# Kernel optimization log

Measured on AMD Instinct MI355X. Metric: run time of the kernel, lower is better.

Reference implementation:

```python
import jax, jax.numpy as jnp
import numpy as np

N = 100000   # n_entity
D = 128      # kg_emb_dim
R = 12       # n_relation
NB = 8       # num_bases
E = 1_000_000
P = 400_000  # hypergraph incidences
HE = 20_000  # hyperedges
B = 64       # users in batch
LR = 64      # related entities per hypergraph per user
LC = 32      # context entities per user
NH = 8       # mha heads
HD = D // NH


def setup_inputs() -> dict:
    key = jax.random.key(0)
    ks = jax.random.split(key, 32)
    s = 1.0 / np.sqrt(D)
    f = lambda i, shape, sc=s: jax.random.normal(ks[i], shape, dtype=jnp.float32) * sc
    ri = lambda i, shape, hi: jax.random.randint(ks[i], shape, 0, hi, dtype=jnp.int32)
    return {
        'entity_emb': f(0, (N, D)),
        'rgcn_bases': f(1, (NB, D, D)),
        'rgcn_comp': f(2, (R, NB)),
        'rgcn_root': f(3, (D, D)),
        'rgcn_bias': jnp.zeros((D,), jnp.float32),
        'sess_theta': f(4, (D, D)),
        'sess_bias': jnp.zeros((D,), jnp.float32),
        'know_theta': f(5, (D, D)),
        'know_bias': jnp.zeros((D,), jnp.float32),
        'in_proj_w': f(6, (3 * D, D)),
        'in_proj_b': jnp.zeros((3 * D,), jnp.float32),
        'out_proj_w': f(7, (D, D)),
        'out_proj_b': jnp.zeros((D,), jnp.float32),
        'attn_his_a': f(8, (D, D)),
        'attn_his_b': f(9, (D, 1)),
        'attn_a': f(10, (D, D)),
        'attn_b': f(11, (D, 1)),
        'rec_bias': jnp.zeros((N,), jnp.float32),
        'edge_src': ri(12, (E,), N),
        'edge_dst': ri(13, (E,), N),
        'edge_type': ri(14, (E,), R),
        'sess_nodes': ri(15, (P,), N),
        'sess_edges': ri(16, (P,), HE),
        'know_nodes': ri(17, (P,), N),
        'know_edges': ri(18, (P,), HE),
        'sess_rel_idx': ri(19, (B, LR), N),
        'know_rel_idx': ri(20, (B, LR), N),
        'context_idx': ri(21, (B, LC), N),
    }


def rgcn_conv(x, bases, comp, root, bias, src, dst, etype):
    # PyG RGCNConv with basis decomposition; per-relation mean aggregation
    # norm = 1/|N_r(i)| : count edges per (dst, relation)
    pair_key = dst * R + etype
    cnt = jax.ops.segment_sum(jnp.ones_like(src, dtype=x.dtype), pair_key, N * R)
    norm = 1.0 / jnp.maximum(cnt[pair_key], 1.0)  # [E]
    w = jnp.einsum('rb,bio->rio', comp, bases)    # [R, D, D]
    out = x @ root + bias
    for r in range(R):
        h_r = x @ w[r]                                            # [N, D]
        coef = norm * (etype == r).astype(x.dtype)                # [E]
        out = out + jax.ops.segment_sum(h_r[src] * coef[:, None], dst, N)
    return out


def hypergraph_conv(x, theta, bias, nodes, edges, n_hyperedges):
    # PyG HypergraphConv (no attention): D^-1 H W B^-1 H^T X Theta + bias
    xt = x @ theta                                                # [N, D]
    ones = jnp.ones(nodes.shape, x.dtype)
    b_deg = jax.ops.segment_sum(ones, edges, n_hyperedges)        # [HE]
    edge_feat = jax.ops.segment_sum(xt[nodes], edges, n_hyperedges)
    edge_feat = edge_feat * jnp.where(b_deg > 0, 1.0 / b_deg, 0.0)[:, None]
    d_deg = jax.ops.segment_sum(ones, nodes, N)                   # [N]
    out = jax.ops.segment_sum(edge_feat[edges], nodes, N)
    return out * jnp.where(d_deg > 0, 1.0 / d_deg, 0.0)[:, None] + bias


def self_attn_batch(h, a, b):
    # SelfAttentionBatch: e = tanh(h a) b; softmax over nodes; weighted sum
    e = jnp.einsum('bld,dk->blk', jnp.tanh(jnp.einsum('bld,de->ble', h, a)), b)[..., 0]
    attn = jax.nn.softmax(e, axis=-1)                             # [B, L]
    return jnp.einsum('bl,bld->bd', attn, h)


def mha(q, kv, in_proj_w, in_proj_b, out_proj_w, out_proj_b):
    # torch.nn.MultiheadAttention (batch_first) math
    wq, wk, wv = in_proj_w[:D], in_proj_w[D:2 * D], in_proj_w[2 * D:]
    bq, bk, bv = in_proj_b[:D], in_proj_b[D:2 * D], in_proj_b[2 * D:]
    qh = (q @ wq.T + bq).reshape(q.shape[0], q.shape[1], NH, HD)
    kh = (kv @ wk.T + bk).reshape(kv.shape[0], kv.shape[1], NH, HD)
    vh = (kv @ wv.T + bv).reshape(kv.shape[0], kv.shape[1], NH, HD)
    logits = jnp.einsum('bqhd,bkhd->bhqk', qh, kh) / np.sqrt(HD)
    attn = jax.nn.softmax(logits, axis=-1)
    o = jnp.einsum('bhqk,bkhd->bqhd', attn, vh).reshape(q.shape[0], q.shape[1], D)
    return o @ out_proj_w.T + out_proj_b


def reference(entity_emb, rgcn_bases, rgcn_comp, rgcn_root, rgcn_bias,
              sess_theta, sess_bias, know_theta, know_bias,
              in_proj_w, in_proj_b, out_proj_w, out_proj_b,
              attn_his_a, attn_his_b, attn_a, attn_b, rec_bias,
              edge_src, edge_dst, edge_type,
              sess_nodes, sess_edges, know_nodes, know_edges,
              sess_rel_idx, know_rel_idx, context_idx):
    # 1) RGCN over the full KG
    kg = rgcn_conv(entity_emb, rgcn_bases, rgcn_comp, rgcn_root, rgcn_bias,
                   edge_src, edge_dst, edge_type)
    # 2) session / knowledge hypergraph convolutions on RGCN output
    sess = hypergraph_conv(kg, sess_theta, sess_bias, sess_nodes, sess_edges, HE)
    know = hypergraph_conv(kg, know_theta, know_bias, know_nodes, know_edges, HE)
    # 3) per-user: related = concat(session_emb, knowledge_emb); context from kg
    related = jnp.concatenate([sess[sess_rel_idx], know[know_rel_idx]], axis=1)  # [B, 2LR, D]
    context = kg[context_idx]                                                    # [B, LC, D]
    # 4) MHItemAttention (context queries related) + gated attention pooling
    att_rel = mha(context, related, in_proj_w, in_proj_b, out_proj_w, out_proj_b)
    his = self_attn_batch(att_rel, attn_his_a, attn_his_b)                       # [B, D]
    user_cat = jnp.concatenate([context, his[:, None, :]], axis=1)               # [B, LC+1, D]
    user = self_attn_batch(user_cat, attn_a, attn_b)                             # [B, D]
    # 5) recommendation scores: F.linear(user, kg_embedding, rec_bias.bias)
    return user @ kg.T + rec_bias                                                # [B, N]
```

## Files before the change

kernel.cpp:

```cpp
#include <hip/hip_runtime.h>
#include <hip/hip_bf16.h>

#define DN 100000
#define DD 128
#define DR 12
#define DNB 8
#define DE 1000000
#define DP 400000
#define DHE 20000
#define DHE2 40000
#define DB 64
#define DLR 64
#define DLC 32
#define DNH 8
#define DHD 16
#define NRBINS (DR * DN)
#define SCAN_CHUNK 1024
#define MCAP 65536

typedef unsigned short ushortT;
typedef unsigned int uintT;
typedef __attribute__((ext_vector_type(8))) short s8v;
typedef __attribute__((ext_vector_type(4))) float f4v;

#define APAD 136

__device__ __forceinline__ ushortT rneb(float v) {
    uintT b = __float_as_uint(v);
    return (ushortT)((b + 0x7FFFu + ((b >> 16) & 1u)) >> 16);
}
__device__ __forceinline__ float b2f(ushortT h) {
    return __uint_as_float(((uintT)h) << 16);
}

__device__ __forceinline__ void split_store8(ushortT* hbase, ushortT* lbase, const float* v)
{
    ushortT h[8], l[8];
    #pragma unroll
    for (int j = 0; j < 8; ++j) {
        h[j] = rneb(v[j]);
        l[j] = rneb(v[j] - b2f(h[j]));
    }
    uint4 hv = make_uint4((uintT)h[0] | ((uintT)h[1] << 16), (uintT)h[2] | ((uintT)h[3] << 16),
                          (uintT)h[4] | ((uintT)h[5] << 16), (uintT)h[6] | ((uintT)h[7] << 16));
    uint4 lv = make_uint4((uintT)l[0] | ((uintT)l[1] << 16), (uintT)l[2] | ((uintT)l[3] << 16),
                          (uintT)l[4] | ((uintT)l[5] << 16), (uintT)l[6] | ((uintT)l[7] << 16));
    *(uint4*)hbase = hv;
    *(uint4*)lbase = lv;
}

__global__ __launch_bounds__(256) void k_presplit_all(
    const float* __restrict__ root, const float* __restrict__ st,
    const float* __restrict__ kt, const float* __restrict__ ipw,
    const float* __restrict__ opw, const float* __restrict__ aha,
    const float* __restrict__ aa, ushortT* __restrict__ outA)
{
    int gid = blockIdx.x * 256 + threadIdx.x;
    int mat = gid >> 14, e = gid & 16383;
    const float* srcs[9] = {root, st, kt, ipw, ipw + 16384, ipw + 32768, opw, aha, aa};
    const float* W = srcs[mat];
    bool t1 = (mat >= 3 && mat <= 6);
    int k = e & 31, n = (e >> 5) & 127, kc = e >> 12;
    float f = t1 ? W[(size_t)n * 128 + kc * 32 + k] : W[(size_t)(kc * 32 + k) * 128 + n];
    ushortT h = rneb(f);
    outA[(size_t)mat * 32768 + e] = h;
    outA[(size_t)mat * 32768 + 16384 + e] = rneb(f - b2f(h));
}

__global__ void k_wcomp_split(const float* __restrict__ comp, const float* __restrict__ bases,
                              ushortT* __restrict__ warena)
{
    int i = blockIdx.x * blockDim.x + threadIdx.x;
    if (i >= DR * DD * DD) return;
    int r = i / (DD * DD), io = i % (DD * DD);
    float s = 0.f;
    #pragma unroll
    for (int b = 0; b < DNB; ++b) s += comp[r * DNB + b] * bases[(size_t)b * DD * DD + io];
    int irow = io >> 7, o = io & 127;
    int kc = irow >> 5, k = irow & 31;
    size_t dst = (size_t)r * 32768 + (size_t)kc * 4096 + o * 32 + k;
    ushortT h = rneb(s);
    warena[dst] = h;
    warena[dst + 16384] = rneb(s - b2f(h));
}

__global__ __launch_bounds__(256) void k_gemm_ds(
    const float* __restrict__ A, const ushortT* __restrict__ Wb,
    const float* __restrict__ bias, const float* __restrict__ rs,
    const int* __restrict__ gidx, float* __restrict__ gout,
    float* __restrict__ C, int M)
{
    __shared__ __align__(16) ushortT Ah[64 * APAD], Al[64 * APAD];
    __shared__ __align__(16) ushortT Bs[8192];
    int tid = threadIdx.x;
    int row0 = blockIdx.x * 64;
    {
        int row = tid >> 2, c0 = (tid & 3) * 32;
        int gr = row0 + row;
        int arow = gr;
        if (gidx && gr < M) arow = gidx[gr];
        const float* ar = A + (size_t)arow * 128 + c0;
        float sc = 1.0f;
        if (rs && gr < M) { float d = rs[gr]; sc = (d > 0.f) ? 1.0f / d : 0.f; }
        #pragma unroll
        for (int g = 0; g < 4; ++g) {
            float v[8] = {};
            if (gr < M) {
                float4 u0 = *(const float4*)(ar + g * 8);
// ... 72 lines not shown
        }
    }
    f4v acc[8] = {};
    int w = tid >> 6, lane = tid & 63, m = lane & 15, quad = lane >> 4;
    for (int kc = 0; kc < 4; ++kc) {
        __syncthreads();
        {
            const ushortT* gh = Wb + kc * 4096;
            const ushortT* gl = Wb + 16384 + kc * 4096;
            *(s8v*)&Bs[tid * 8]        = *(const s8v*)&gh[tid * 8];
            *(s8v*)&Bs[2048 + tid * 8] = *(const s8v*)&gh[2048 + tid * 8];
            *(s8v*)&Bs[4096 + tid * 8] = *(const s8v*)&gl[tid * 8];
            *(s8v*)&Bs[6144 + tid * 8] = *(const s8v*)&gl[2048 + tid * 8];
        }
        __syncthreads();
        s8v ah = *(const s8v*)&Ah[(w * 16 + m) * APAD + kc * 32 + quad * 8];
        s8v al = *(const s8v*)&Al[(w * 16 + m) * APAD + kc * 32 + quad * 8];
        #pragma unroll
        for (int nt = 0; nt < 8; ++nt) {
            int boff = (nt * 16 + m) * 32 + quad * 8;
            s8v bh = *(const s8v*)&Bs[boff];
            s8v bl = *(const s8v*)&Bs[4096 + boff];
            acc[nt] = __builtin_amdgcn_mfma_f32_16x16x32_bf16(ah, bh, acc[nt], 0, 0, 0);
            acc[nt] = __builtin_amdgcn_mfma_f32_16x16x32_bf16(al, bh, acc[nt], 0, 0, 0);
            acc[nt] = __builtin_amdgcn_mfma_f32_16x16x32_bf16(ah, bl, acc[nt], 0, 0, 0);
        }
    }
    float bv[8];
    #pragma unroll
    for (int nt = 0; nt < 8; ++nt) bv[nt] = bvec[nt * 16 + m];
    #pragma unroll
    for (int rr = 0; rr < 4; ++rr) {
        float p = 0.f;
        #pragma unroll
        for (int nt = 0; nt < 8; ++nt) p += tanhf(acc[nt][rr]) * bv[nt];
        #pragma unroll
        for (int o = 1; o < 16; o <<= 1) p += __shfl_xor(p, o);
        int gr = row0 + w * 16 + quad * 4 + rr;
        if (m == 0 && gr < M) e[gr] = p;
    }
}

template <int L>
__global__ __launch_bounds__(128) void k_pool_apply(const float* __restrict__ h,
                                                    const float* __restrict__ e,
                                                    float* __restrict__ out,
                                                    ushortT* __restrict__ us)
{
    __shared__ float es[L];
    int b = blockIdx.x, tid = threadIdx.x;
    if (tid < L) es[tid] = e[b * L + tid];
    __syncthreads();
    float mx = -1e30f;
    #pragma unroll
    for (int l = 0; l < L; ++l) mx = fmaxf(mx, es[l]);
    float wgt[L];
    float sum = 0.f;
    #pragma unroll
    for (int l = 0; l < L; ++l) { wgt[l] = __expf(es[l] - mx); sum += wgt[l]; }
    float inv = 1.0f / sum;
    float o = 0.f;
    #pragma unroll
    for (int l = 0; l < L; ++l) o += wgt[l] * h[((size_t)b * L + l) * 128 + tid];
    float val = o * inv;
    out[(size_t)b * 128 + tid] = val;
    if (us) {
        ushortT hh = rneb(val);
        ushortT ll = rneb(val - b2f(hh));
        int e_ = ((tid >> 5) * 2048) + b * 32 + (tid & 31);
        us[e_] = hh;
        us[8192 + e_] = ll;
    }
}

__global__ void k_build_ucat(const float* __restrict__ ctx, const float* __restrict__ his,
                             float* ucat)
{
    int i = blockIdx.x * blockDim.x + threadIdx.x;
    if (i >= DB * 33 * 128) return;
    int d = i & 127, l = (i >> 7) % 33, b = i / (33 * 128);
    ucat[i] = (l < 32) ? ctx[((size_t)b * 32 + l) * 128 + d] : his[(size_t)b * 128 + d];
}

__global__ __launch_bounds__(256) void k_rgcn_all(
    const float* __restrict__ x, const ushortT* __restrict__ warena,
    const int* __restrict__ seglist, const int* __restrict__ soff,
    const int* __restrict__ slen, const int* __restrict__ ssrc,
    const int* __restrict__ stypebase, const int* __restrict__ bo,
    float* __restrict__ kg)
{
    __shared__ __align__(16) ushortT Ah[64 * APAD], Al[64 * APAD];
    __shared__ __align__(16) ushortT Bs[8192];
    int bid = blockIdx.x;
    if (bid >= bo[DR]) return;
    int r = 0;
    #pragma unroll 1
    while (bid >= bo[r + 1]) ++r;
    int s0 = stypebase[r], s1 = stypebase[r + 1];
    int base = s0 + (bid - bo[r]) * 64;
    int nrow = min(64, s1 - base);
    int tid = threadIdx.x;
    const ushortT* Wb = warena + (size_t)r * 32768;
    {
        int row = tid >> 2, c0 = (tid & 3) * 32;
        float a[32] = {};
        if (row < nrow) {
            int key = seglist[base + row];
            int len = slen[key];
            int st = soff[key] - len;
            for (int i = 0; i < len; ++i) {
                const float* xr = x + (size_t)ssrc[st + i] * 128 + c0;
                #pragma unroll
                for (int j = 0; j < 8; ++j) {
                    float4 v = *(const float4*)(xr + j * 4);
                    a[j*4+0] += v.x; a[j*4+1] += v.y; a[j*4+2] += v.z; a[j*4+3] += v.w;
                }
            }
            float inv = 1.0f / (float)max(len, 1);
            #pragma unroll
            for (int j = 0; j < 32; ++j) a[j] *= inv;
        }
        #pragma unroll
        for (int g = 0; g < 4; ++g)
            split_store8(&Ah[row * APAD + c0 + g * 8], &Al[row * APAD + c0 + g * 8], a + g * 8);
    }
    f4v acc[8] = {};
    int w = tid >> 6, lane = tid & 63, m = lane & 15, quad = lane >> 4;
    for (int kc = 0; kc < 4; ++kc) {
        __syncthreads();
        {
            const ushortT* gh = Wb + kc * 4096;
            const ushortT* gl = Wb + 16384 + kc * 4096;
            *(s8v*)&Bs[tid * 8]        = *(const s8v*)&gh[tid * 8];
            *(s8v*)&Bs[2048 + tid * 8] = *(const s8v*)&gh[2048 + tid * 8];
            *(s8v*)&Bs[4096 + tid * 8] = *(const s8v*)&gl[tid * 8];
            *(s8v*)&Bs[6144 + tid * 8] = *(const s8v*)&gl[2048 + tid * 8];
        }
        __syncthreads();
        s8v ah = *(const s8v*)&Ah[(w * 16 + m) * APAD + kc * 32 + quad * 8];
        s8v al = *(const s8v*)&Al[(w * 16 + m) * APAD + kc * 32 + quad * 8];
        #pragma unroll
        for (int nt = 0; nt < 8; ++nt) {
            int boff = (nt * 16 + m) * 32 + quad * 8;
            s8v bh = *(const s8v*)&Bs[boff];
            s8v bl = *(const s8v*)&Bs[4096 + boff];
            acc[nt] = __builtin_amdgcn_mfma_f32_16x16x32_bf16(ah, bh, acc[nt], 0, 0, 0);
            acc[nt] = __builtin_amdgcn_mfma_f32_16x16x32_bf16(al, bh, acc[nt], 0, 0, 0);
            acc[nt] = __builtin_amdgcn_mfma_f32_16x16x32_bf16(ah, bl, acc[nt], 0, 0, 0);
        }
    }
    #pragma unroll
    for (int rr = 0; rr < 4; ++rr) {
        int rt = w * 16 + quad * 4 + rr;
        if (rt < nrow) {
            int dst = seglist[base + rt] - r * DN;
            float* kr = kg + (size_t)dst * 128 + m;
            #pragma unroll
            for (int nt = 0; nt < 8; ++nt)
                atomicAdd(&kr[nt * 16], acc[nt][rr]);
        }
    }
}

__global__ __launch_bounds__(256) void k_score_ds(
    const float* __restrict__ kg, const ushortT* __restrict__ Ub,
    const float* __restrict__ rb, float* __restrict__ out)
{
    __shared__ __align__(16) ushortT Ah[64 * APAD], Al[64 * APAD];
    __shared__ __align__(16) ushortT Bs[4096];
    int tid = threadIdx.x;
    int n0 = blockIdx.x * 64;
    {
        int row = tid >> 2, c0 = (tid & 3) * 32;
        int gr = n0 + row;
        const float* ar = kg + (size_t)gr * 128 + c0;
        #pragma unroll
        for (int g = 0; g < 4; ++g) {
            float v[8] = {};
            if (gr < DN) {
                float4 u0 = *(const float4*)(ar + g * 8);
                float4 u1 = *(const float4*)(ar + g * 8 + 4);
                v[0]=u0.x; v[1]=u0.y; v[2]=u0.z; v[3]=u0.w;
                v[4]=u1.x; v[5]=u1.y; v[6]=u1.z; v[7]=u1.w;
            }
            split_store8(&Ah[row * APAD + c0 + g * 8], &Al[row * APAD + c0 + g * 8], v);
        }
    }
    f4v acc[4] = {};
    int w = tid >> 6, lane = tid & 63, m = lane & 15, quad = lane >> 4;
    for (int kc = 0; kc < 4; ++kc) {
        __syncthreads();
        {
            const ushortT* gh = Ub + kc * 2048;
            const ushortT* gl = Ub + 8192 + kc * 2048;
            *(s8v*)&Bs[tid * 8]        = *(const s8v*)&gh[tid * 8];
            *(s8v*)&Bs[2048 + tid * 8] = *(const s8v*)&gl[tid * 8];
        }
        __syncthreads();
        s8v ah = *(const s8v*)&Ah[(w * 16 + m) * APAD + kc * 32 + quad * 8];
        s8v al = *(const s8v*)&Al[(w * 16 + m) * APAD + kc * 32 + quad * 8];
        #pragma unroll
        for (int nt = 0; nt < 4; ++nt) {
            int boff = (nt * 16 + m) * 32 + quad * 8;
            s8v bh = *(const s8v*)&Bs[boff];
            s8v bl = *(const s8v*)&Bs[2048 + boff];
            acc[nt] = __builtin_amdgcn_mfma_f32_16x16x32_bf16(ah, bh, acc[nt], 0, 0, 0);
            acc[nt] = __builtin_amdgcn_mfma_f32_16x16x32_bf16(al, bh, acc[nt], 0, 0, 0);
            acc[nt] = __builtin_amdgcn_mfma_f32_16x16x32_bf16(ah, bl, acc[nt], 0, 0, 0);
        }
    }
    int n = n0 + w * 16 + quad * 4;
    if (n < DN) {
        float4 rbv = *(const float4*)&rb[n];
        #pragma unroll
        for (int nt = 0; nt < 4; ++nt) {
            int b = nt * 16 + m;
            float4 o = make_float4(acc[nt][0] + rbv.x, acc[nt][1] + rbv.y,
                                   acc[nt][2] + rbv.z, acc[nt][3] + rbv.w);
            *(float4*)&out[(size_t)b * DN + n] = o;
        }
    }
}

__global__ void k_scan_pass1(const int* __restrict__ in, int n, int* __restrict__ bsum)
{
    __shared__ int red[256];
    int b = blockIdx.x, t = threadIdx.x;
    int i0 = b * SCAN_CHUNK + t * 4;
    int s = 0;
    #pragma unroll
    for (int j = 0; j < 4; ++j) {
        int i = i0 + j;
        if (i < n) s += in[i];
    }
    red[t] = s;
    __syncthreads();
    for (int o = 128; o > 0; o >>= 1) {
        if (t < o) red[t] += red[t + o];
        __syncthreads();
    }
    if (t == 0) bsum[b] = red[0];
}

__global__ __launch_bounds__(256) void k_scan_pass2p(int* bsum, int nb, int* total)
{
    __shared__ int lds[256];
    __shared__ int carry;
    int t = threadIdx.x;
    if (t == 0) carry = 0;
    __syncthreads();
    for (int c0 = 0; c0 < nb; c0 += 256) {
        int i = c0 + t;
        int v = (i < nb) ? bsum[i] : 0;
        lds[t] = v;
        __syncthreads();
        for (int o = 1; o < 256; o <<= 1) {
            int add = (t >= o) ? lds[t - o] : 0;
            __syncthreads();
            lds[t] += add;
            __syncthreads();
        }
        int myc = carry;
        if (i < nb) bsum[i] = lds[t] - v + myc;
        int tot = lds[255];
        __syncthreads();
        if (t == 0) carry = myc + tot;
        __syncthreads();
    }
    if (total && t == 0) *total = carry;
}

__global__ void k_scan_pass3(const int* __restrict__ in, int n, const int* __restrict__ bsum,
                             int* __restrict__ out)
{
    __shared__ int lds[256];
    int b = blockIdx.x, t = threadIdx.x;
    int i0 = b * SCAN_CHUNK + t * 4;
    int v[4]; int s = 0;
    #pragma unroll
    for (int j = 0; j < 4; ++j) {
        int i = i0 + j;
        int x = 0;
        if (i < n) x = in[i];
        v[j] = x; s += x;
    }
    lds[t] = s;
    __syncthreads();
    for (int o = 1; o < 256; o <<= 1) {
        int add = (t >= o) ? lds[t - o] : 0;
        __syncthreads();
        lds[t] += add;
        __syncthreads();
    }
    int run = lds[t] - s + bsum[b];
    #pragma unroll
    for (int j = 0; j < 4; ++j) {
        int i = i0 + j;
        if (i < n) { out[i] = run; run += v[j]; }
    }
}

__global__ void k_scan2_pass1(const int* __restrict__ in, int n, int* bV, int* bP)
{
    __shared__ int redV[256], redP[256];
    int b = blockIdx.x, t = threadIdx.x;
    int i0 = b * SCAN_CHUNK + t * 4;
    int sv = 0, sp = 0;
    #pragma unroll
    for (int j = 0; j < 4; ++j) {
        int i = i0 + j;
        if (i < n) { int v = in[i]; sv += v; sp += (v > 0); }
    }
    redV[t] = sv; redP[t] = sp;
    __syncthreads();
    for (int o = 128; o > 0; o >>= 1) {
        if (t < o) { redV[t] += redV[t + o]; redP[t] += redP[t + o]; }
        __syncthreads();
    }
    if (t == 0) { bV[b] = redV[0]; bP[b] = redP[0]; }
}

__global__ __launch_bounds__(256) void k_scan2_pass2(int* bV, int* bP, int nb, int* totalP)
{
    __shared__ int lds[256];
    __shared__ int carry;
    int t = threadIdx.x;
    #pragma unroll 1
    for (int which = 0; which < 2; ++which) {
        int* bsum = which ? bP : bV;
        __syncthreads();
        if (t == 0) carry = 0;
        __syncthreads();
        for (int c0 = 0; c0 < nb; c0 += 256) {
            int i = c0 + t;
            int v = (i < nb) ? bsum[i] : 0;
            lds[t] = v;
            __syncthreads();
            for (int o = 1; o < 256; o <<= 1) {
                int add = (t >= o) ? lds[t - o] : 0;
                __syncthreads();
                lds[t] += add;
                __syncthreads();
            }
            int myc = carry;
            if (i < nb) bsum[i] = lds[t] - v + myc;
            int tot = lds[255];
            __syncthreads();
            if (t == 0) carry = myc + tot;
            __syncthreads();
        }
        if (which == 1 && totalP && t == 0) *totalP = carry;
    }
}

__global__ void k_scan2_pass3(const int* __restrict__ in, int n,
                              const int* __restrict__ bV, const int* __restrict__ bP,
                              int* __restrict__ outV, int* __restrict__ outP)
{
    __shared__ int ldsV[256], ldsP[256];
    int b = blockIdx.x, t = threadIdx.x;
    int i0 = b * SCAN_CHUNK + t * 4;
    int v[4]; int sv = 0, sp = 0;
    #pragma unroll
    for (int j = 0; j < 4; ++j) {
        int i = i0 + j;
        int x = 0;
        if (i < n) x = in[i];
        v[j] = x; sv += x; sp += (x > 0);
    }
    ldsV[t] = sv; ldsP[t] = sp;
    __syncthreads();
    for (int o = 1; o < 256; o <<= 1) {
        int addV = (t >= o) ? ldsV[t - o] : 0;
        int addP = (t >= o) ? ldsP[t - o] : 0;
        __syncthreads();
        ldsV[t] += addV; ldsP[t] += addP;
        __syncthreads();
    }
    int runV = ldsV[t] - sv + bV[b];
    int runP = ldsP[t] - sp + bP[b];
    #pragma unroll
    for (int j = 0; j < 4; ++j) {
        int i = i0 + j;
        if (i < n) {
            outV[i] = runV; outP[i] = runP;
            runV += v[j]; runP += (v[j] > 0);
        }
    }
}

__global__ void k_hist_both(const int* __restrict__ dst, const int* __restrict__ et,
                            int* __restrict__ hist,
                            const int* __restrict__ se, const int* __restrict__ ke,
                            int* __restrict__ hhist)
{
    int i = blockIdx.x * blockDim.x + threadIdx.x;
    if (i < DE) {
        atomicAdd(&hist[(size_t)et[i] * DN + dst[i]], 1);
    } else {
        int j = i - DE;
        if (j < DP) atomicAdd(&hhist[se[j]], 1);
        else if (j < 2 * DP) atomicAdd(&hhist[DHE + ke[j - DP]], 1);
    }
}

__global__ void k_seglist(const int* __restrict__ hist, const int* __restrict__ segpos,
                          int* __restrict__ seglist, int n)
{
    int i = blockIdx.x * blockDim.x + threadIdx.x;
    if (i < n && hist[i] > 0) seglist[segpos[i]] = i;
}

__global__ void k_stypebase(const int* __restrict__ segpos, int* stybase, int* bo)
{
    int t = threadIdx.x;
    if (t < DR) stybase[t] = segpos[(size_t)t * DN];
    if (t == 0) {
        int acc = 0; bo[0] = 0;
        int prev = segpos[0];
        for (int r = 0; r < DR; ++r) {
            int nxt = (r == DR - 1) ? stybase[DR] : segpos[(size_t)(r + 1) * DN];
            acc += (nxt - prev + 63) >> 6;
            bo[r + 1] = acc;
            prev = nxt;
        }
    }
}

__global__ void k_bucket_both(const int* __restrict__ src, const int* __restrict__ dst,
                              const int* __restrict__ et, int* __restrict__ soff,
                              int* __restrict__ ssrc,
                              const int* __restrict__ sn, const int* __restrict__ se,
                              const int* __restrict__ kn, const int* __restrict__ ke,
                              int* __restrict__ hoff, int* __restrict__ pns)
{
    int i = blockIdx.x * blockDim.x + threadIdx.x;
    if (i < DE) {
        int key = et[i] * DN + dst[i];
        int pos = atomicAdd(&soff[key], 1);
        ssrc[pos] = src[i];
    } else {
        int j = i - DE;
        if (j >= 2 * DP) return;
        int e, node;
        if (j < DP) { e = se[j]; node = sn[j]; }
        else { e = DHE + ke[j - DP]; node = kn[j - DP]; }
        int pos = atomicAdd(&hoff[e], 1);
        pns[pos] = node;
    }
}

__global__ void k_hyper_agg(const float* __restrict__ xsrc, const int* __restrict__ pns,
                            const int* __restrict__ hoff, const int* __restrict__ hcnt,
                            const int* __restrict__ heneed, float* __restrict__ efeat)
{
    int lane = threadIdx.x & 63;
    int he = (blockIdx.x * blockDim.x + threadIdx.x) >> 6;
    if (he >= DHE2) return;
    if (!heneed[he]) return;
    int len = hcnt[he];
    int st = hoff[he] - len;
    int half = lane >> 5;
    int c16 = (lane & 31) * 4;
    float4 acc = make_float4(0.f, 0.f, 0.f, 0.f);
    int c = 0;
    for (; c + 4 <= len; c += 4) {
        int n0 = pns[st + c + half];
        int n1 = pns[st + c + 2 + half];
        float4 v0 = *(const float4*)&xsrc[(size_t)n0 * 128 + c16];
        float4 v1 = *(const float4*)&xsrc[(size_t)n1 * 128 + c16];
        acc.x += v0.x + v1.x; acc.y += v0.y + v1.y;
        acc.z += v0.z + v1.z; acc.w += v0.w + v1.w;
    }
    for (; c < len; c += 2) {
        int idx = c + half;
        if (idx < len) {
            int n = pns[st + idx];
            float4 v = *(const float4*)&xsrc[(size_t)n * 128 + c16];
            acc.x += v.x; acc.y += v.y; acc.z += v.z; acc.w += v.w;
        }
    }
    acc.x += __shfl_xor(acc.x, 32);
    acc.y += __shfl_xor(acc.y, 32);
    acc.z += __shfl_xor(acc.z, 32);
    acc.w += __shfl_xor(acc.w, 32);
    if (half == 0) {
        float inv = (len > 0) ? 1.0f / (float)len : 0.f;
        float4 o = make_float4(acc.x * inv, acc.y * inv, acc.z * inv, acc.w * inv);
        *(float4*)&efeat[(size_t)he * 128 + c16] = o;
    }
}

__global__ void k_slot_assign2(const int* __restrict__ sidx, const int* __restrict__ kidx,
                               int* slot_s, int* slot_k, int* scnt)
{
    int i = blockIdx.x * blockDim.x + threadIdx.x;
    if (i < DB * DLR) {
        int node = sidx[i];
        if (atomicCAS(&slot_s[node], -1, -2) == -1) slot_s[node] = atomicAdd(&scnt[0], 1);
    } else if (i < 2 * DB * DLR) {
        int node = kidx[i - DB * DLR];
        if (atomicCAS(&slot_k[node], -1, -2) == -1) slot_k[node] = atomicAdd(&scnt[1], 1);
    }
}

__global__ __launch_bounds__(256) void k_sdeg_match(
    const int* __restrict__ nodes, const int* __restrict__ he, const int* __restrict__ slot,
    float* sdeg, int* mcnt, int* mhe, int* msl, int* heneed, int heBase)
{
    __shared__ int lcnt, lbase;
    if (threadIdx.x == 0) lcnt = 0;
    __syncthreads();
    int i = blockIdx.x * 256 + threadIdx.x;
    int s = -1, lidx = 0, h = 0;
    if (i < DP) {
        s = slot[nodes[i]];
        if (s >= 0) {
            h = heBase + he[i];
            heneed[h] = 1;
            atomicAdd(&sdeg[s], 1.0f);
            lidx = atomicAdd(&lcnt, 1);
        }
    }
    __syncthreads();
    if (threadIdx.x == 0) lbase = (lcnt > 0) ? atomicAdd(mcnt, lcnt) : 0;
    __syncthreads();
    if (s >= 0) {
        int idx = lbase + lidx;
        if (idx < MCAP) { mhe[idx] = h; msl[idx] = s; }
    }
}

__global__ void k_accmatch2(const float* __restrict__ efeat,
                            const int* __restrict__ mhe_s, const int* __restrict__ msl_s,
                            const int* __restrict__ mhe_k, const int* __restrict__ msl_k,
                            const int* __restrict__ mcnt,
                            float* sacc_s, float* sacc_k)
{
    int lane = threadIdx.x & 63;
    int w = (blockIdx.x * blockDim.x + threadIdx.x) >> 6;
    int nw = (gridDim.x * blockDim.x) >> 6;
    int Ms = min(mcnt[0], MCAP), Mk = min(mcnt[1], MCAP);
    for (int i = w; i < Ms + Mk; i += nw) {
        bool sess = i < Ms;
// ... 42 lines not shown
        Qs[q][d] = qb[((size_t)b * 32 + q) * 128 + h * 16 + d] * 0.25f;
    }
    __syncthreads();
    int q = tid >> 3;
    int jg = tid & 7;
    float lg[16];
    float m = -1e30f;
    #pragma unroll
    for (int jj = 0; jj < 16; ++jj) {
        int j = jg * 16 + jj;
        float s = 0.f;
        #pragma unroll
        for (int d = 0; d < 16; ++d) s += Qs[q][d] * Ks[j][d];
        lg[jj] = s;
        m = fmaxf(m, s);
    }
    #pragma unroll
    for (int o = 1; o < 8; o <<= 1) m = fmaxf(m, __shfl_xor(m, o));
    float sum = 0.f;
    float acc[16] = {};
    #pragma unroll
    for (int jj = 0; jj < 16; ++jj) {
        float p = __expf(lg[jj] - m);
        sum += p;
        int j = jg * 16 + jj;
        #pragma unroll
        for (int d = 0; d < 16; ++d) acc[d] += p * Vs[j][d];
    }
    #pragma unroll
    for (int o = 1; o < 8; o <<= 1) {
        sum += __shfl_xor(sum, o);
        #pragma unroll
        for (int d = 0; d < 16; ++d) acc[d] += __shfl_xor(acc[d], o);
    }
    if (jg == 0) {
        float inv = 1.0f / sum;
        #pragma unroll
        for (int d = 0; d < 16; ++d)
            ob[((size_t)b * 32 + q) * 128 + h * 16 + d] = acc[d] * inv;
    }
}

extern "C" void kernel_launch(void* const* d_in, const int* in_sizes, int n_in,
                              void* d_out, int out_size, void* d_ws, size_t ws_size,
                              hipStream_t stream)
{
    const float* emb        = (const float*)d_in[0];
    const float* bases      = (const float*)d_in[1];
    const float* comp       = (const float*)d_in[2];
    const float* root       = (const float*)d_in[3];
    const float* rgcn_bias  = (const float*)d_in[4];
    const float* sess_theta = (const float*)d_in[5];
    const float* sess_bias  = (const float*)d_in[6];
    const float* know_theta = (const float*)d_in[7];
    const float* know_bias  = (const float*)d_in[8];
    const float* in_proj_w  = (const float*)d_in[9];
    const float* in_proj_b  = (const float*)d_in[10];
    const float* out_proj_w = (const float*)d_in[11];
    const float* out_proj_b = (const float*)d_in[12];
    const float* attn_his_a = (const float*)d_in[13];
    const float* attn_his_b = (const float*)d_in[14];
    const float* attn_a     = (const float*)d_in[15];
    const float* attn_b     = (const float*)d_in[16];
    const float* rec_bias   = (const float*)d_in[17];
    const int* edge_src     = (const int*)d_in[18];
    const int* edge_dst     = (const int*)d_in[19];
    const int* edge_type    = (const int*)d_in[20];
    const int* sess_nodes   = (const int*)d_in[21];
    const int* sess_edges   = (const int*)d_in[22];
    const int* know_nodes   = (const int*)d_in[23];
    const int* know_edges   = (const int*)d_in[24];
    const int* sess_rel_idx = (const int*)d_in[25];
    const int* know_rel_idx = (const int*)d_in[26];
    const int* context_idx  = (const int*)d_in[27];
    float* out = (float*)d_out;

    float* wsf = (float*)d_ws;
    size_t off = 0;
    auto alloc = [&](size_t n) { size_t r = off; off += (n + 255) & ~(size_t)255; return r; };
    float* kg      = wsf + alloc(12800000);
    float* tmp     = wsf + alloc(12800000);
    ushortT* warena = (ushortT*)(wsf + alloc(196608));
    int*   bsumV   = (int*)(wsf + alloc(2048));
    int*   bsumP   = (int*)(wsf + alloc(2048));
    int*   stybase = (int*)(wsf + alloc(16));
    int*   bo      = (int*)(wsf + alloc(16));
    size_t zstart = off;
    int*   hhist   = (int*)(wsf + alloc(DHE2));
    int*   heneed  = (int*)(wsf + alloc(DHE2));
    int*   mcnt    = (int*)(wsf + alloc(16));
    int*   scnt    = (int*)(wsf + alloc(16));
    float* sdeg_s  = wsf + alloc(4096);
    float* sdeg_k  = wsf + alloc(4096);
    float* sacc_s  = wsf + alloc(524288);
    float* sacc_k  = wsf + alloc(524288);
    size_t zend = off;
    size_t fstart = off;
    int*   slot_s  = (int*)(wsf + alloc(100000));
    int*   slot_k  = (int*)(wsf + alloc(100000));
    size_t fend = off;
    int*   hoff    = (int*)(wsf + alloc(DHE2));
    int*   pns     = (int*)(wsf + alloc(2 * DP));
    int*   mhe_s   = (int*)(wsf + alloc(MCAP));
    int*   msl_s   = (int*)(wsf + alloc(MCAP));
    int*   mhe_k   = (int*)(wsf + alloc(MCAP));
    int*   msl_k   = (int*)(wsf + alloc(MCAP));
    float* so_s    = wsf + alloc(524288);
    float* so_k    = wsf + alloc(524288);
    float* related = wsf + alloc(1048576);
    float* ctx     = wsf + alloc(262144);
    float* qb      = wsf + alloc(262144);
    float* kb      = wsf + alloc(1048576);
    float* vb      = wsf + alloc(1048576);
    float* obuf    = wsf + alloc(262144);
    float* attrel  = wsf + alloc(262144);
    float* his     = wsf + alloc(8192);
    float* ucat    = wsf + alloc(270336);
    float* userb   = wsf + alloc(8192);
    float* e1      = wsf + alloc(2048);
    float* e2      = wsf + alloc(2112);
    (void)ws_size; (void)in_sizes; (void)n_in; (void)out_size;

    int*   hist    = (int*)tmp;
    int*   soff    = (int*)tmp + 1200000;
    int*   segpos  = (int*)tmp + 2400000;
    int*   seglist = (int*)tmp + 3600000;
    int*   ssrc    = (int*)tmp + 4800000;
    float* efeat   = tmp + 6000000;
    ushortT* wsplit = (ushortT*)(tmp + 12200000);
    ushortT* usplit = (ushortT*)(tmp + 12400000);

    const int nbR = (NRBINS + SCAN_CHUNK - 1) / SCAN_CHUNK;
    const int nbH = (DHE2 + SCAN_CHUNK - 1) / SCAN_CHUNK;

    hipMemsetAsync(wsf + zstart, 0, (zend - zstart) * 4, stream);
    hipMemsetAsync(wsf + fstart, 0xFF, (fend - fstart) * 4, stream);
    hipMemsetAsync(hist, 0, (size_t)NRBINS * 4, stream);

    k_presplit_all<<<576, 256, 0, stream>>>(root, sess_theta, know_theta, in_proj_w,
                                            out_proj_w, attn_his_a, attn_a, wsplit);

    k_slot_assign2<<<32, 256, 0, stream>>>(sess_rel_idx, know_rel_idx, slot_s, slot_k, scnt);
    k_sdeg_match<<<(DP + 255) / 256, 256, 0, stream>>>(sess_nodes, sess_edges, slot_s,
                                                       sdeg_s, mcnt, mhe_s, msl_s, heneed, 0);
    k_sdeg_match<<<(DP + 255) / 256, 256, 0, stream>>>(know_nodes, know_edges, slot_k,
                                                       sdeg_k, mcnt + 1, mhe_k, msl_k, heneed, DHE);

    k_hist_both<<<(DE + 2 * DP + 255) / 256, 256, 0, stream>>>(edge_dst, edge_type, hist,
                                                               sess_edges, know_edges, hhist);
    k_scan2_pass1<<<nbR, 256, 0, stream>>>(hist, NRBINS, bsumV, bsumP);
    k_scan2_pass2<<<1, 256, 0, stream>>>(bsumV, bsumP, nbR, stybase + DR);
    k_scan2_pass3<<<nbR, 256, 0, stream>>>(hist, NRBINS, bsumV, bsumP, soff, segpos);
    k_scan_pass1<<<nbH, 256, 0, stream>>>(hhist, DHE2, bsumV);
    k_scan_pass2p<<<1, 256, 0, stream>>>(bsumV, nbH, nullptr);
    k_scan_pass3<<<nbH, 256, 0, stream>>>(hhist, DHE2, bsumV, hoff);

    k_stypebase<<<1, 64, 0, stream>>>(segpos, stybase, bo);
    k_seglist<<<(NRBINS + 255) / 256, 256, 0, stream>>>(hist, segpos, seglist, NRBINS);

    k_bucket_both<<<(DE + 2 * DP + 255) / 256, 256, 0, stream>>>(
        edge_src, edge_dst, edge_type, soff, ssrc,
        sess_nodes, sess_edges, know_nodes, know_edges, hoff, pns);

    k_wcomp_split<<<(DR * DD * DD + 255) / 256, 256, 0, stream>>>(comp, bases, warena);

    int gemmN = (DN + 63) / 64;
    k_gemm_ds<<<gemmN, 256, 0, stream>>>(emb, wsplit + 0 * 32768, rgcn_bias, nullptr,
                                         nullptr, nullptr, kg, DN);
    k_rgcn_all<<<(DE + 63) / 64 + DR, 256, 0, stream>>>(emb, warena, seglist, soff, hist,
                                                        ssrc, stybase, bo, kg);

    k_hyper_agg<<<(DHE2 * 64 + 255) / 256, 256, 0, stream>>>(kg, pns, hoff, hhist, heneed, efeat);
    k_accmatch2<<<256, 256, 0, stream>>>(efeat, mhe_s, msl_s, mhe_k, msl_k, mcnt, sacc_s, sacc_k);

    k_gemm_ds<<<64, 256, 0, stream>>>(sacc_s, wsplit + 1 * 32768, sess_bias, sdeg_s,
                                      nullptr, nullptr, so_s, 4096);
    k_gemm_ds<<<64, 256, 0, stream>>>(sacc_k, wsplit + 2 * 32768, know_bias, sdeg_k,
                                      nullptr, nullptr, so_k, 4096);
    k_rel_gather2<<<(2 * DB * DLR * 32 + 255) / 256, 256, 0, stream>>>(
        so_s, so_k, slot_s, slot_k, sess_rel_idx, know_rel_idx, related);

    k_gemm_ds<<<(DB * DLC + 63) / 64, 256, 0, stream>>>(kg, wsplit + 3 * 32768,
                                                        in_proj_b, nullptr,
                                                        context_idx, ctx, qb, DB * DLC);
    k_gemm_ds<<<(DB * 128 + 63) / 64, 256, 0, stream>>>(related, wsplit + 4 * 32768,
                                                        in_proj_b + DD, nullptr,
                                                        nullptr, nullptr, kb, DB * 128);
    k_gemm_ds<<<(DB * 128 + 63) / 64, 256, 0, stream>>>(related, wsplit + 5 * 32768,
                                                        in_proj_b + 2 * DD, nullptr,
                                                        nullptr, nullptr, vb, DB * 128);
    k_mha<<<DB * DNH, 256, 0, stream>>>(qb, kb, vb, obuf);
    k_gemm_ds<<<(DB * DLC + 63) / 64, 256, 0, stream>>>(obuf, wsplit + 6 * 32768,
                                                        out_proj_b, nullptr,
                                                        nullptr, nullptr, attrel, DB * DLC);

    k_tanh_dot_ds<<<(DB * DLC + 63) / 64, 256, 0, stream>>>(attrel, wsplit + 7 * 32768,
                                                            attn_his_b, e1, DB * DLC);
    k_pool_apply<32><<<DB, 128, 0, stream>>>(attrel, e1, his, nullptr);
    k_build_ucat<<<(DB * 33 * 128 + 255) / 256, 256, 0, stream>>>(ctx, his, ucat);
    k_tanh_dot_ds<<<(DB * 33 + 63) / 64, 256, 0, stream>>>(ucat, wsplit + 8 * 32768,
                                                           attn_b, e2, DB * 33);
    k_pool_apply<33><<<DB, 128, 0, stream>>>(ucat, e2, userb, usplit);
    k_score_ds<<<gemmN, 256, 0, stream>>>(kg, usplit, rec_bias, out);
}
```

Measured before the change: 968.1 us.

## Fuse RGCN root GEMM and per-relation aggregation into one dst-tiled kernel

Reorders the edge bucketing key to dst-major (dst*R+type) so each 64-destination tile owns a contiguous edge range. A single kernel then computes the root transform plus all 12 relation transforms for that tile, accumulating in registers and writing kg directly with bias. This replaces the global float atomics into kg and the separate root GEMM. It also merges the hypergraph histogram and scan into the same bin array, which drops the dual scan, seglist and stypebase kernels. In exchange, each block loops over 13 phases with LDS atomics and a tag-scan over all of the tile's edges every phase. It falls back to per-row gathering when a tile has more than 1024 edges.

Measured after the change: 1.985 ms. 105% more time.

```diff
diff --git a/kernel.cpp b/kernel.cpp
--- a/kernel.cpp
+++ b/kernel.cpp
@@ -15,8 +15,10 @@
 #define DNH 8
 #define DHD 16
 #define NRBINS (DR * DN)
+#define NALLBINS (NRBINS + DHE2)
 #define SCAN_CHUNK 1024
 #define MCAP 65536
+#define RNECAP 1024
 
 typedef unsigned short ushortT;
 typedef unsigned int uintT;
@@ -24,6 +26,7 @@
 typedef __attribute__((ext_vector_type(4))) float f4v;
 
 #define APAD 136
+#define AFS 130
 
 __device__ __forceinline__ ushortT rneb(float v) {
     uintT b = __float_as_uint(v);
@@ -262,82 +265,134 @@
     ucat[i] = (l < 32) ? ctx[((size_t)b * 32 + l) * 128 + d] : his[(size_t)b * 128 + d];
 }
 
-__global__ __launch_bounds__(256) void k_rgcn_all(
-    const float* __restrict__ x, const ushortT* __restrict__ warena,
-    const int* __restrict__ seglist, const int* __restrict__ soff,
-    const int* __restrict__ slen, const int* __restrict__ ssrc,
-    const int* __restrict__ stypebase, const int* __restrict__ bo,
-    float* __restrict__ kg)
-{
-    __shared__ __align__(16) ushortT Ah[64 * APAD], Al[64 * APAD];
+__global__ __launch_bounds__(256) void k_rgcn_fused(
+    const float* __restrict__ x, const ushortT* __restrict__ rootsplit,
+    const ushortT* __restrict__ warena, const float* __restrict__ bias,
+    const int* __restrict__ soff, const int* __restrict__ hist,
+    const int* __restrict__ ssrc, float* __restrict__ kg)
+{
+    __shared__ __align__(16) float U[64 * APAD / 2 * 2];
     __shared__ __align__(16) ushortT Bs[8192];
-    int bid = blockIdx.x;
-    if (bid >= bo[DR]) return;
-    int r = 0;
-    #pragma unroll 1
-    while (bid >= bo[r + 1]) ++r;
-    int s0 = stypebase[r], s1 = stypebase[r + 1];
-    int base = s0 + (bid - bo[r]) * 64;
-    int nrow = min(64, s1 - base);
+    __shared__ ushortT rowr[RNECAP];
+    ushortT* Ah = (ushortT*)U;
+    ushortT* Al = (ushortT*)U + 64 * APAD;
     int tid = threadIdx.x;
-    const ushortT* Wb = warena + (size_t)r * 32768;
-    {
-        int row = tid >> 2, c0 = (tid & 3) * 32;
-        float a[32] = {};
-        if (row < nrow) {
-            int key = seglist[base + row];
-            int len = slen[key];
-            int st = soff[key] - len;
-            for (int i = 0; i < len; ++i) {
-                const float* xr = x + (size_t)ssrc[st + i] * 128 + c0;
+    int dst0 = blockIdx.x * 64;
+    int nrow = min(64, DN - dst0);
+    int kfirst = dst0 * DR;
+    int klast  = (dst0 + nrow) * DR - 1;
+    int st0 = soff[kfirst] - hist[kfirst];
+    int ne  = soff[klast] - st0;
+    bool fb = (ne > RNECAP);
+    int w = tid >> 6, lane = tid & 63, m = lane & 15, quad = lane >> 4;
+    int row = tid >> 2, c0 = (tid & 3) * 32;
+    f4v acc[8] = {};
+
+    if (!fb) {
+        for (int kk = tid; kk < nrow * DR; kk += 256) {
+            int key = kfirst + kk;
+            int len = hist[key];
+            int st = soff[key] - len - st0;
+            ushortT tag = (ushortT)(((kk / DR) << 4) | (kk % DR));
+            for (int i = 0; i < len; ++i) rowr[st + i] = tag;
+        }
+    }
+
+    for (int p = 0; p < 13; ++p) {
+        __syncthreads();
+        if (p == 0) {
+            float a[32] = {};
+            if (row < nrow) {
+                const float* ar = x + (size_t)(dst0 + row) * 128 + c0;
                 #pragma unroll
                 for (int j = 0; j < 8; ++j) {
-                    float4 v = *(const float4*)(xr + j * 4);
-                    a[j*4+0] += v.x; a[j*4+1] += v.y; a[j*4+2] += v.z; a[j*4+3] += v.w;
+                    float4 v = *(const float4*)(ar + j * 4);
+                    a[j*4+0]=v.x; a[j*4+1]=v.y; a[j*4+2]=v.z; a[j*4+3]=v.w;
                 }
             }
-            float inv = 1.0f / (float)max(len, 1);
             #pragma unroll
-            for (int j = 0; j < 32; ++j) a[j] *= inv;
-        }
-        #pragma unroll
-        for (int g = 0; g < 4; ++g)
-            split_store8(&Ah[row * APAD + c0 + g * 8], &Al[row * APAD + c0 + g * 8], a + g * 8);
-    }
-    f4v acc[8] = {};
-    int w = tid >> 6, lane = tid & 63, m = lane & 15, quad = lane >> 4;
-    for (int kc = 0; kc < 4; ++kc) {
-        __syncthreads();
-        {
+            for (int g = 0; g < 4; ++g)
+                split_store8(&Ah[row * APAD + c0 + g * 8], &Al[row * APAD + c0 + g * 8], a + g * 8);
+        } else if (!fb) {
+            int r = p - 1;
+            for (int i = tid; i < 64 * AFS; i += 256) U[i] = 0.f;
+            __syncthreads();
+            for (int t = tid; t < ne * 64; t += 256) {
+                int e = t >> 6;
+                ushortT tg = rowr[e];
+                if ((tg & 15) != r) continue;
+                int rw = tg >> 4, c = t & 63;
+                int src = ssrc[st0 + e];
+                float2 v = *(const float2*)&x[(size_t)src * 128 + c * 2];
+                atomicAdd(&U[rw * AFS + c * 2 + 0], v.x);
+                atomicAdd(&U[rw * AFS + c * 2 + 1], v.y);
+            }
+            __syncthreads();
+            int len = (row < nrow) ? hist[(dst0 + row) * DR + r] : 0;
+            float inv = (len > 0) ? 1.0f / (float)len : 0.f;
+            float a[32];
+            #pragma unroll
+            for (int j = 0; j < 32; ++j) a[j] = U[row * AFS + c0 + j] * inv;
+            __syncthreads();
+            #pragma unroll
+            for (int g = 0; g < 4; ++g)
+                split_store8(&Ah[row * APAD + c0 + g * 8], &Al[row * APAD + c0 + g * 8], a + g * 8);
+        } else {
+            int r = p - 1;
+            float a[32] = {};
+            if (row < nrow) {
+                int key = (dst0 + row) * DR + r;
+                int len = hist[key];
+                int st = soff[key] - len;
+                for (int i = 0; i < len; ++i) {
+                    const float* xr = x + (size_t)ssrc[st + i] * 128 + c0;
+                    #pragma unroll
+                    for (int j = 0; j < 8; ++j) {
+                        float4 v = *(const float4*)(xr + j * 4);
+                        a[j*4+0]+=v.x; a[j*4+1]+=v.y; a[j*4+2]+=v.z; a[j*4+3]+=v.w;
+                    }
+                }
+                float inv = (len > 0) ? 1.0f / (float)len : 0.f;
+                #pragma unroll
+                for (int j = 0; j < 32; ++j) a[j] *= inv;
+            }
+            #pragma unroll
+            for (int g = 0; g < 4; ++g)
+                split_store8(&Ah[row * APAD + c0 + g * 8], &Al[row * APAD + c0 + g * 8], a + g * 8);
+        }
+        const ushortT* Wb = (p == 0) ? rootsplit : warena + (size_t)(p - 1) * 32768;
+        for (int kc = 0; kc < 4; ++kc) {
+            __syncthreads();
             const ushortT* gh = Wb + kc * 4096;
             const ushortT* gl = Wb + 16384 + kc * 4096;
             *(s8v*)&Bs[tid * 8]        = *(const s8v*)&gh[tid * 8];
             *(s8v*)&Bs[2048 + tid * 8] = *(const s8v*)&gh[2048 + tid * 8];
             *(s8v*)&Bs[4096 + tid * 8] = *(const s8v*)&gl[tid * 8];
             *(s8v*)&Bs[6144 + tid * 8] = *(const s8v*)&gl[2048 + tid * 8];
-        }
-        __syncthreads();
-        s8v ah = *(const s8v*)&Ah[(w * 16 + m) * APAD + kc * 32 + quad * 8];
-        s8v al = *(const s8v*)&Al[(w * 16 + m) * APAD + kc * 32 + quad * 8];
-        #pragma unroll
-        for (int nt = 0; nt < 8; ++nt) {
-            int boff = (nt * 16 + m) * 32 + quad * 8;
-            s8v bh = *(const s8v*)&Bs[boff];
-            s8v bl = *(const s8v*)&Bs[4096 + boff];
-            acc[nt] = __builtin_amdgcn_mfma_f32_16x16x32_bf16(ah, bh, acc[nt], 0, 0, 0);
-            acc[nt] = __builtin_amdgcn_mfma_f32_16x16x32_bf16(al, bh, acc[nt], 0, 0, 0);
-            acc[nt] = __builtin_amdgcn_mfma_f32_16x16x32_bf16(ah, bl, acc[nt], 0, 0, 0);
-        }
-    }
+            __syncthreads();
+            s8v ah = *(const s8v*)&Ah[(w * 16 + m) * APAD + kc * 32 + quad * 8];
+            s8v al = *(const s8v*)&Al[(w * 16 + m) * APAD + kc * 32 + quad * 8];
+            #pragma unroll
+            for (int nt = 0; nt < 8; ++nt) {
+                int boff = (nt * 16 + m) * 32 + quad * 8;
+                s8v bh = *(const s8v*)&Bs[boff];
+                s8v bl = *(const s8v*)&Bs[4096 + boff];
+                acc[nt] = __builtin_amdgcn_mfma_f32_16x16x32_bf16(ah, bh, acc[nt], 0, 0, 0);
+                acc[nt] = __builtin_amdgcn_mfma_f32_16x16x32_bf16(al, bh, acc[nt], 0, 0, 0);
+                acc[nt] = __builtin_amdgcn_mfma_f32_16x16x32_bf16(ah, bl, acc[nt], 0, 0, 0);
+            }
+        }
+    }
+    float bv[8];
+    #pragma unroll
+    for (int nt = 0; nt < 8; ++nt) bv[nt] = bias[nt * 16 + m];
     #pragma unroll
     for (int rr = 0; rr < 4; ++rr) {
-        int rt = w * 16 + quad * 4 + rr;
-        if (rt < nrow) {
-            int dst = seglist[base + rt] - r * DN;
-            float* kr = kg + (size_t)dst * 128 + m;
+        int gr = dst0 + w * 16 + quad * 4 + rr;
+        if (gr < DN) {
             #pragma unroll
             for (int nt = 0; nt < 8; ++nt)
-                atomicAdd(&kr[nt * 16], acc[nt][rr]);
+                kg[(size_t)gr * 128 + nt * 16 + m] = acc[nt][rr] + bv[nt];
         }
     }
 }
@@ -480,130 +535,17 @@
     }
 }
 
-__global__ void k_scan2_pass1(const int* __restrict__ in, int n, int* bV, int* bP)
-{
-    __shared__ int redV[256], redP[256];
-    int b = blockIdx.x, t = threadIdx.x;
-    int i0 = b * SCAN_CHUNK + t * 4;
-    int sv = 0, sp = 0;
-    #pragma unroll
-    for (int j = 0; j < 4; ++j) {
-        int i = i0 + j;
-        if (i < n) { int v = in[i]; sv += v; sp += (v > 0); }
-    }
-    redV[t] = sv; redP[t] = sp;
-    __syncthreads();
-    for (int o = 128; o > 0; o >>= 1) {
-        if (t < o) { redV[t] += redV[t + o]; redP[t] += redP[t + o]; }
-        __syncthreads();
-    }
-    if (t == 0) { bV[b] = redV[0]; bP[b] = redP[0]; }
-}
-
-__global__ __launch_bounds__(256) void k_scan2_pass2(int* bV, int* bP, int nb, int* totalP)
-{
-    __shared__ int lds[256];
-    __shared__ int carry;
-    int t = threadIdx.x;
-    #pragma unroll 1
-    for (int which = 0; which < 2; ++which) {
-        int* bsum = which ? bP : bV;
-        __syncthreads();
-        if (t == 0) carry = 0;
-        __syncthreads();
-        for (int c0 = 0; c0 < nb; c0 += 256) {
-            int i = c0 + t;
-            int v = (i < nb) ? bsum[i] : 0;
-            lds[t] = v;
-            __syncthreads();
-            for (int o = 1; o < 256; o <<= 1) {
-                int add = (t >= o) ? lds[t - o] : 0;
-                __syncthreads();
-                lds[t] += add;
-                __syncthreads();
-            }
-            int myc = carry;
-            if (i < nb) bsum[i] = lds[t] - v + myc;
-            int tot = lds[255];
-            __syncthreads();
-            if (t == 0) carry = myc + tot;
-            __syncthreads();
-        }
-        if (which == 1 && totalP && t == 0) *totalP = carry;
-    }
-}
-
-__global__ void k_scan2_pass3(const int* __restrict__ in, int n,
-                              const int* __restrict__ bV, const int* __restrict__ bP,
-                              int* __restrict__ outV, int* __restrict__ outP)
-{
-    __shared__ int ldsV[256], ldsP[256];
-    int b = blockIdx.x, t = threadIdx.x;
-    int i0 = b * SCAN_CHUNK + t * 4;
-    int v[4]; int sv = 0, sp = 0;
-    #pragma unroll
-    for (int j = 0; j < 4; ++j) {
-        int i = i0 + j;
-        int x = 0;
-        if (i < n) x = in[i];
-        v[j] = x; sv += x; sp += (x > 0);
-    }
-    ldsV[t] = sv; ldsP[t] = sp;
-    __syncthreads();
-    for (int o = 1; o < 256; o <<= 1) {
-        int addV = (t >= o) ? ldsV[t - o] : 0;
-        int addP = (t >= o) ? ldsP[t - o] : 0;
-        __syncthreads();
-        ldsV[t] += addV; ldsP[t] += addP;
-        __syncthreads();
-    }
-    int runV = ldsV[t] - sv + bV[b];
-    int runP = ldsP[t] - sp + bP[b];
-    #pragma unroll
-    for (int j = 0; j < 4; ++j) {
-        int i = i0 + j;
-        if (i < n) {
-            outV[i] = runV; outP[i] = runP;
-            runV += v[j]; runP += (v[j] > 0);
-        }
-    }
-}
-
 __global__ void k_hist_both(const int* __restrict__ dst, const int* __restrict__ et,
                             int* __restrict__ hist,
-                            const int* __restrict__ se, const int* __restrict__ ke,
-                            int* __restrict__ hhist)
+                            const int* __restrict__ se, const int* __restrict__ ke)
 {
     int i = blockIdx.x * blockDim.x + threadIdx.x;
     if (i < DE) {
-        atomicAdd(&hist[(size_t)et[i] * DN + dst[i]], 1);
+        atomicAdd(&hist[dst[i] * DR + et[i]], 1);
     } else {
         int j = i - DE;
-        if (j < DP) atomicAdd(&hhist[se[j]], 1);
-        else if (j < 2 * DP) atomicAdd(&hhist[DHE + ke[j - DP]], 1);
-    }
-}
-
-__global__ void k_seglist(const int* __restrict__ hist, const int* __restrict__ segpos,
-                          int* __restrict__ seglist, int n)
-{
-    int i = blockIdx.x * blockDim.x + threadIdx.x;
-    if (i < n && hist[i] > 0) seglist[segpos[i]] = i;
-}
-
-__global__ void k_stypebase(const int* __restrict__ segpos, int* stybase, int* bo)
-{
-    int t = threadIdx.x;
-    if (t < DR) stybase[t] = segpos[(size_t)t * DN];
-    if (t == 0) {
-        int acc = 0; bo[0] = 0;
-        int prev = segpos[0];
-        for (int r = 0; r < DR; ++r) {
-            int nxt = (r == DR - 1) ? stybase[DR] : segpos[(size_t)(r + 1) * DN];
-            acc += (nxt - prev + 63) >> 6;
-            bo[r + 1] = acc;
-            prev = nxt;
-        }
+        if (j < DP) atomicAdd(&hist[NRBINS + se[j]], 1);
+        else if (j < 2 * DP) atomicAdd(&hist[NRBINS + DHE + ke[j - DP]], 1);
     }
 }
 
@@ -612,11 +554,11 @@
                               int* __restrict__ ssrc,
                               const int* __restrict__ sn, const int* __restrict__ se,
                               const int* __restrict__ kn, const int* __restrict__ ke,
-                              int* __restrict__ hoff, int* __restrict__ pns)
+                              int* __restrict__ pns)
 {
     int i = blockIdx.x * blockDim.x + threadIdx.x;
     if (i < DE) {
-        int key = et[i] * DN + dst[i];
+        int key = dst[i] * DR + et[i];
         int pos = atomicAdd(&soff[key], 1);
         ssrc[pos] = src[i];
     } else {
@@ -625,8 +567,8 @@
         int e, node;
         if (j < DP) { e = se[j]; node = sn[j]; }
         else { e = DHE + ke[j - DP]; node = kn[j - DP]; }
-        int pos = atomicAdd(&hoff[e], 1);
-        pns[pos] = node;
+        int pos = atomicAdd(&soff[NRBINS + e], 1);
+        pns[pos - DE] = node;
     }
 }
 
@@ -639,7 +581,7 @@
     if (he >= DHE2) return;
     if (!heneed[he]) return;
     int len = hcnt[he];
-    int st = hoff[he] - len;
+    int st = hoff[he] - len - DE;
     int half = lane >> 5;
     int c16 = (lane & 31) * 4;
     float4 acc = make_float4(0.f, 0.f, 0.f, 0.f);
@@ -848,11 +790,7 @@
     float* tmp     = wsf + alloc(12800000);
     ushortT* warena = (ushortT*)(wsf + alloc(196608));
     int*   bsumV   = (int*)(wsf + alloc(2048));
-    int*   bsumP   = (int*)(wsf + alloc(2048));
-    int*   stybase = (int*)(wsf + alloc(16));
-    int*   bo      = (int*)(wsf + alloc(16));
     size_t zstart = off;
-    int*   hhist   = (int*)(wsf + alloc(DHE2));
     int*   heneed  = (int*)(wsf + alloc(DHE2));
     int*   mcnt    = (int*)(wsf + alloc(16));
     int*   scnt    = (int*)(wsf + alloc(16));
@@ -865,7 +803,6 @@
     int*   slot_s  = (int*)(wsf + alloc(100000));
     int*   slot_k  = (int*)(wsf + alloc(100000));
     size_t fend = off;
-    int*   hoff    = (int*)(wsf + alloc(DHE2));
     int*   pns     = (int*)(wsf + alloc(2 * DP));
     int*   mhe_s   = (int*)(wsf + alloc(MCAP));
     int*   msl_s   = (int*)(wsf + alloc(MCAP));
@@ -888,20 +825,17 @@
     (void)ws_size; (void)in_sizes; (void)n_in; (void)out_size;
 
     int*   hist    = (int*)tmp;
-    int*   soff    = (int*)tmp + 1200000;
-    int*   segpos  = (int*)tmp + 2400000;
-    int*   seglist = (int*)tmp + 3600000;
-    int*   ssrc    = (int*)tmp + 4800000;
-    float* efeat   = tmp + 6000000;
+    int*   soff    = (int*)tmp + 1240000;
+    int*   ssrc    = (int*)tmp + 2480000;
+    float* efeat   = tmp + 3600000;
     ushortT* wsplit = (ushortT*)(tmp + 12200000);
     ushortT* usplit = (ushortT*)(tmp + 12400000);
 
-    const int nbR = (NRBINS + SCAN_CHUNK - 1) / SCAN_CHUNK;
-    const int nbH = (DHE2 + SCAN_CHUNK - 1) / SCAN_CHUNK;
+    const int nbA = (NALLBINS + SCAN_CHUNK - 1) / SCAN_CHUNK;
 
     hipMemsetAsync(wsf + zstart, 0, (zend - zstart) * 4, stream);
     hipMemsetAsync(wsf + fstart, 0xFF, (fend - fstart) * 4, stream);
-    hipMemsetAsync(hist, 0, (size_t)NRBINS * 4, stream);
+    hipMemsetAsync(hist, 0, (size_t)NALLBINS * 4, stream);
 
     k_presplit_all<<<576, 256, 0, stream>>>(root, sess_theta, know_theta, in_proj_w,
                                             out_proj_w, attn_his_a, attn_a, wsplit);
@@ -913,30 +847,22 @@
                                                        sdeg_k, mcnt + 1, mhe_k, msl_k, heneed, DHE);
 
     k_hist_both<<<(DE + 2 * DP + 255) / 256, 256, 0, stream>>>(edge_dst, edge_type, hist,
-                                                               sess_edges, know_edges, hhist);
-    k_scan2_pass1<<<nbR, 256, 0, stream>>>(hist, NRBINS, bsumV, bsumP);
-    k_scan2_pass2<<<1, 256, 0, stream>>>(bsumV, bsumP, nbR, stybase + DR);
-    k_scan2_pass3<<<nbR, 256, 0, stream>>>(hist, NRBINS, bsumV, bsumP, soff, segpos);
-    k_scan_pass1<<<nbH, 256, 0, stream>>>(hhist, DHE2, bsumV);
-    k_scan_pass2p<<<1, 256, 0, stream>>>(bsumV, nbH, nullptr);
-    k_scan_pass3<<<nbH, 256, 0, stream>>>(hhist, DHE2, bsumV, hoff);
-
-    k_stypebase<<<1, 64, 0, stream>>>(segpos, stybase, bo);
-    k_seglist<<<(NRBINS + 255) / 256, 256, 0, stream>>>(hist, segpos, seglist, NRBINS);
-
+                                                               sess_edges, know_edges);
+    k_scan_pass1<<<nbA, 256, 0, stream>>>(hist, NALLBINS, bsumV);
+    k_scan_pass2p<<<1, 256, 0, stream>>>(bsumV, nbA, nullptr);
+    k_scan_pass3<<<nbA, 256, 0, stream>>>(hist, NALLBINS, bsumV, soff);
     k_bucket_both<<<(DE + 2 * DP + 255) / 256, 256, 0, stream>>>(
         edge_src, edge_dst, edge_type, soff, ssrc,
-        sess_nodes, sess_edges, know_nodes, know_edges, hoff, pns);
+        sess_nodes, sess_edges, know_nodes, know_edges, pns);
 
     k_wcomp_split<<<(DR * DD * DD + 255) / 256, 256, 0, stream>>>(comp, bases, warena);
 
     int gemmN = (DN + 63) / 64;
-    k_gemm_ds<<<gemmN, 256, 0, stream>>>(emb, wsplit + 0 * 32768, rgcn_bias, nullptr,
-                                         nullptr, nullptr, kg, DN);
-    k_rgcn_all<<<(DE + 63) / 64 + DR, 256, 0, stream>>>(emb, warena, seglist, soff, hist,
-                                                        ssrc, stybase, bo, kg);
-
-    k_hyper_agg<<<(DHE2 * 64 + 255) / 256, 256, 0, stream>>>(kg, pns, hoff, hhist, heneed, efeat);
+    k_rgcn_fused<<<gemmN, 256, 0, stream>>>(emb, wsplit + 0 * 32768, warena, rgcn_bias,
+                                            soff, hist, ssrc, kg);
+
+    k_hyper_agg<<<(DHE2 * 64 + 255) / 256, 256, 0, stream>>>(kg, pns, soff + NRBINS,
+                                                             hist + NRBINS, heneed, efeat);
     k_accmatch2<<<256, 256, 0, stream>>>(efeat, mhe_s, msl_s, mhe_k, msl_k, mcnt, sacc_s, sacc_k);
 
     k_gemm_ds<<<64, 256, 0, stream>>>(sacc_s, wsplit + 1 * 32768, sess_bias, sdeg_s,
```
